# Optimization experiments

Measured on AMD Instinct MI355X. Metric: run time of the kernel, lower is better.

The kernel has to match this reference:

```python
import jax, jax.numpy as jnp
import numpy as np

HEADS = 8
DIM_HEAD = 32


def setup_inputs() -> dict:
    key = jax.random.key(0)
    k1, k2, k3 = jax.random.split(key, 3)
    dim = 256
    hd = HEADS * DIM_HEAD  # 256
    x = jax.random.normal(k1, (2, dim, 16, 64, 64), dtype=jnp.float32)
    w_qkv = jax.random.normal(k2, (3 * hd, dim), dtype=jnp.float32) * (1.0 / np.sqrt(dim))
    w_out = jax.random.normal(k3, (dim, hd), dtype=jnp.float32) * (1.0 / np.sqrt(hd))
    b_out = jnp.zeros((dim,), dtype=jnp.float32)
    return {"x": x, "w_qkv": w_qkv, "w_out": w_out, "b_out": b_out}


def reference(x, w_qkv, w_out, b_out):
    b, c, f, h, w = x.shape
    n = h * w
    scale = DIM_HEAD ** (-0.5)
    # (b c f h w) -> ((b f) c (h w))
    xr = jnp.transpose(x, (0, 2, 1, 3, 4)).reshape(b * f, c, n)
    # 1x1 conv (no bias) == channel GEMM
    qkv = jnp.einsum('oc,bcn->bon', w_qkv, xr)  # (bf, 3*H*D, n)
    q, k, v = jnp.split(qkv, 3, axis=1)
    def heads(t):
        return t.reshape(b * f, HEADS, DIM_HEAD, n)
    q, k, v = heads(q), heads(k), heads(v)
    q = jax.nn.softmax(q, axis=-2) * scale   # softmax over feature dim d
    k = jax.nn.softmax(k, axis=-1)           # softmax over spatial dim n
    context = jnp.einsum('bhdn,bhen->bhde', k, v)   # (bf, H, D, D)
    out = jnp.einsum('bhde,bhdn->bhen', context, q)  # (bf, H, D, n)
    out = out.reshape(b * f, HEADS * DIM_HEAD, n)
    out = jnp.einsum('oc,bcn->bon', w_out, out) + b_out[None, :, None]
    # ((b f) c (h w)) -> (b c f h w)
    out = out.reshape(b, f, c, h, w)
    return jnp.transpose(out, (0, 2, 1, 3, 4))
```

## Files before the change

kernel.cpp:

```cpp
#include <hip/hip_runtime.h>
#include <cmath>


typedef unsigned short u16;
typedef __attribute__((ext_vector_type(4))) unsigned short u16x4;
typedef __attribute__((ext_vector_type(8))) unsigned short u16x8;
typedef __attribute__((ext_vector_type(4))) unsigned int   u32x4;
typedef __attribute__((ext_vector_type(8))) short bf16x8;
typedef __attribute__((ext_vector_type(4))) float f32x4;

#define XCH_STRIDE 65536
#define XB_STRIDE  16777216

__device__ __forceinline__ float bf2f(u16 u) {
    union { unsigned int i; float f; } w; w.i = ((unsigned int)u) << 16; return w.f;
}
__device__ __forceinline__ u16 f2bf(float f) {
    union { float f; unsigned int i; } w; w.f = f;
    return (u16)((w.i + 0x7FFFu + ((w.i >> 16) & 1u)) >> 16);
}
__device__ __forceinline__ void async16(const void* g, void* l) {
    __builtin_amdgcn_global_load_lds(
        (const __attribute__((address_space(1))) unsigned int*)g,
        (__attribute__((address_space(3))) unsigned int*)l, 16, 0, 0);
}

__global__ __launch_bounds__(256) void k_cvt_x(const float* __restrict__ x,
                                               u16* __restrict__ xbf, int fr0)
{
    const int tid = threadIdx.x;
    const int n0 = blockIdx.x * 64;
    const int c0 = blockIdx.y * 64;
    const int fl = blockIdx.z;
    const int frame = fr0 + fl, b = frame >> 4, f = frame & 15;
    const float* xb = x + (size_t)b * XB_STRIDE + (size_t)f * 4096;
    __shared__ float T[64][65];
    const int nn = tid & 63, cq = tid >> 6;
    #pragma unroll
    for (int r = 0; r < 16; ++r) {
        const int cl = r * 4 + cq;
        T[cl][nn] = xb[(size_t)(c0 + cl) * XCH_STRIDE + n0 + nn];
    }
    __syncthreads();
    const int jl = tid >> 2, c16 = (tid & 3) * 16;
    u16* dst = xbf + ((size_t)fl * 4096 + n0 + jl) * 256 + c0 + c16;
    u16x8 a, bv;
    #pragma unroll
    for (int i = 0; i < 8; ++i) a[i] = f2bf(T[c16 + i][jl]);
    #pragma unroll
    for (int i = 0; i < 8; ++i) bv[i] = f2bf(T[c16 + 8 + i][jl]);
    *(u16x8*)dst = a;
    *(u16x8*)(dst + 8) = bv;
}

__global__ __launch_bounds__(256) void k_cvt_w(const float* __restrict__ w,
                                               u16* __restrict__ wbf)
{
    const int i = (blockIdx.x * 256 + threadIdx.x) * 8;
    u16x8 o;
    #pragma unroll
    for (int j = 0; j < 8; ++j) o[j] = f2bf(w[i + j]);
    *(u16x8*)(wbf + i) = o;
}

__global__ __launch_bounds__(256) void k_qkv_mfma(const u16* __restrict__ xbf,
                                                  const u16* __restrict__ wq,
                                                  u16* __restrict__ qkv)
{
    const int tid = threadIdx.x;
    const int lane = tid & 63, wave = tid >> 6;
    const int ln = lane & 15, quad = lane >> 4;
    const int wm = wave & 1, wn = wave >> 1;
    const int j0 = blockIdx.x * 128;
    const int o0 = blockIdx.y * 128;

    __shared__ __align__(16) u16 sm[128 * 136];
    u16* As = sm;
    u16* Bs = sm + 4096;

    f32x4 acc[4][4] = {};
    const int lrow = lane >> 2;
    const int lk8 = (lane & 3) * 8;

    for (int kk = 0; kk < 256; kk += 32) {
        __syncthreads();
        #pragma unroll
        for (int p = 0; p < 2; ++p) {
            const int chunk = wave * 2 + p;
            const int r = chunk * 16 + lrow;
            async16(wq  + (size_t)(o0 + r) * 256 + kk + lk8, As + chunk * 512);
            async16(xbf + (size_t)(j0 + r) * 256 + kk + lk8, Bs + chunk * 512);
        }
        __syncthreads();
        bf16x8 af[4], bfv[4];
        #pragma unroll
        for (int mi = 0; mi < 4; ++mi)
            af[mi] = *(const bf16x8*)&As[(wm * 64 + mi * 16 + ln) * 32 + quad * 8];
        #pragma unroll
        for (int ni = 0; ni < 4; ++ni)
            bfv[ni] = *(const bf16x8*)&Bs[(wn * 64 + ni * 16 + ln) * 32 + quad * 8];
        #pragma unroll
        for (int mi = 0; mi < 4; ++mi)
            #pragma unroll
            for (int ni = 0; ni < 4; ++ni)
                acc[mi][ni] = __builtin_amdgcn_mfma_f32_16x16x32_bf16(
                    af[mi], bfv[ni], acc[mi][ni], 0, 0, 0);
    }

    __syncthreads();
    u16* outl = sm;
    #pragma unroll
    for (int mi = 0; mi < 4; ++mi)
        #pragma unroll
        for (int ni = 0; ni < 4; ++ni) {
            const int jl = wn * 64 + ni * 16 + ln;
            const int ob = wm * 64 + mi * 16 + quad * 4;
            u16x4 u;
            u[0] = f2bf(acc[mi][ni][0]); u[1] = f2bf(acc[mi][ni][1]);
            u[2] = f2bf(acc[mi][ni][2]); u[3] = f2bf(acc[mi][ni][3]);
            *(u16x4*)&outl[jl * 136 + ob] = u;
        }
    __syncthreads();
    #pragma unroll
    for (int r = 0; r < 8; ++r) {
        const int row = r * 16 + (tid >> 4);
        const int cb = (tid & 15) * 8;
        u32x4 v = *(const u32x4*)&outl[row * 136 + cb];
        *(u32x4*)(qkv + (size_t)(j0 + row) * 768 + o0 + cb) = v;
    }
}

__global__ __launch_bounds__(256) void k_softmax_k(u16* __restrict__ qkv)
{
    const int h = blockIdx.x, fl = blockIdx.y;
    const int tid = threadIdx.x;
    u16* base = qkv + (size_t)fl * 4096 * 768 + 256 + h * 32;
    const int d4 = (tid & 7) * 4, jj = tid >> 3;

    __shared__ float red[32 * 33 + 32];
    float* Lm  = red;
    float* Rsc = red + 32 * 33;

    float m[4] = {-1e30f, -1e30f, -1e30f, -1e30f};
    for (int it = 0; it < 128; ++it) {
        const u16x4 u = *(const u16x4*)(base + (size_t)(jj + it * 32) * 768 + d4);
        #pragma unroll
        for (int i = 0; i < 4; ++i) m[i] = fmaxf(m[i], bf2f(u[i]));
    }
    #pragma unroll
    for (int i = 0; i < 4; ++i) Lm[jj * 33 + d4 + i] = m[i];
    __syncthreads();
    if (tid < 32) {
        float M = -1e30f;
        for (int k = 0; k < 32; ++k) M = fmaxf(M, Lm[k * 33 + tid]);
        Rsc[tid] = M;
    }
    __syncthreads();
    float Mv[4];
    #pragma unroll
    for (int i = 0; i < 4; ++i) Mv[i] = Rsc[d4 + i];
    __syncthreads();

    float s[4] = {0.f, 0.f, 0.f, 0.f};
    for (int it = 0; it < 128; ++it) {
        const u16x4 u = *(const u16x4*)(base + (size_t)(jj + it * 32) * 768 + d4);
        #pragma unroll
        for (int i = 0; i < 4; ++i) s[i] += __expf(bf2f(u[i]) - Mv[i]);
    }
    #pragma unroll
    for (int i = 0; i < 4; ++i) Lm[jj * 33 + d4 + i] = s[i];
    __syncthreads();
    if (tid < 32) {
        float S = 0.f;
        for (int k = 0; k < 32; ++k) S += Lm[k * 33 + tid];
        Rsc[tid] = 1.0f / S;
    }
    __syncthreads();
    float Iv[4];
    #pragma unroll
    for (int i = 0; i < 4; ++i) Iv[i] = Rsc[d4 + i];

    for (int it = 0; it < 128; ++it) {
        u16* p = base + (size_t)(jj + it * 32) * 768 + d4;
        u16x4 u = *(const u16x4*)p;
        u16x4 o;
        #pragma unroll
        for (int i = 0; i < 4; ++i) o[i] = f2bf(__expf(bf2f(u[i]) - Mv[i]) * Iv[i]);
        *(u16x4*)p = o;
    }
}

__global__ __launch_bounds__(256) void k_softmax_q(u16* __restrict__ qkv)
{
    const int tid = threadIdx.x;
    const int j = blockIdx.x * 32 + (tid >> 3);
    const int h = tid & 7;
    u16* p = qkv + (size_t)j * 768 + h * 32;
    u16x8 u[4];
    #pragma unroll
    for (int g = 0; g < 4; ++g) u[g] = *(const u16x8*)(p + g * 8);
    float v[32];
    float m = -1e30f;
    #pragma unroll
    for (int g = 0; g < 4; ++g)
        #pragma unroll
        for (int i = 0; i < 8; ++i) { v[g * 8 + i] = bf2f(u[g][i]); m = fmaxf(m, v[g * 8 + i]); }
    float s = 0.f;
    #pragma unroll
    for (int i = 0; i < 32; ++i) { v[i] = __expf(v[i] - m); s += v[i]; }
    const float inv = 0.17677669529663687f / s;
    #pragma unroll
    for (int g = 0; g < 4; ++g) {
        u16x8 o;
        #pragma unroll
        for (int i = 0; i < 8; ++i) o[i] = f2bf(v[g * 8 + i] * inv);
        *(u16x8*)(p + g * 8) = o;
    }
}

__global__ __launch_bounds__(256) void k_context_w2(const u16* __restrict__ qkv,
                                                    const float* __restrict__ w_out,
                                                    u16* __restrict__ w2)
{
    const int h = blockIdx.x, fl = blockIdx.y;
    const int tid = threadIdx.x;
    __shared__ float Ks[64 * 36], Vs[64 * 36], Cs[32 * 33];

    const int d = tid >> 3, e4 = (tid & 7) * 4;
    const int lr = tid >> 2, lc8 = (tid & 3) * 8;
    float acc[4] = {0.f, 0.f, 0.f, 0.f};
    const u16* kcol = qkv + (size_t)fl * 4096 * 768 + 256 + h * 32 + lc8;

    for (int jt = 0; jt < 4096; jt += 64) {
        const u16* kp = kcol + (size_t)(jt + lr) * 768;
        u16x8 ku = *(const u16x8*)kp;
        u16x8 vu = *(const u16x8*)(kp + 256);
        __syncthreads();
        #pragma unroll
        for (int i = 0; i < 8; ++i) {
            Ks[lr * 36 + lc8 + i] = bf2f(ku[i]);
            Vs[lr * 36 + lc8 + i] = bf2f(vu[i]);
        }
        __syncthreads();
        #pragma unroll 8
        for (int jr = 0; jr < 64; ++jr) {
            const float kd = Ks[jr * 36 + d];
            const f32x4 vv = *(const f32x4*)&Vs[jr * 36 + e4];
            acc[0] = fmaf(kd, vv[0], acc[0]);
            acc[1] = fmaf(kd, vv[1], acc[1]);
            acc[2] = fmaf(kd, vv[2], acc[2]);
            acc[3] = fmaf(kd, vv[3], acc[3]);
        }
    }
    __syncthreads();
    #pragma unroll
    for (int i = 0; i < 4; ++i) Cs[d * 33 + e4 + i] = acc[i];
    __syncthreads();

    const int o = tid;
    float a2[32];
    #pragma unroll
    for (int dd = 0; dd < 32; ++dd) a2[dd] = 0.f;
    for (int e = 0; e < 32; ++e) {
        const float wv = w_out[(size_t)o * 256 + h * 32 + e];
        #pragma unroll
        for (int dd = 0; dd < 32; ++dd) a2[dd] = fmaf(wv, Cs[dd * 33 + e], a2[dd]);
    }
    u16* wp = w2 + (size_t)fl * 65536 + (size_t)o * 256 + h * 32;
    #pragma unroll
    for (int g = 0; g < 4; ++g) {
        u16x8 ov;
        #pragma unroll
        for (int i = 0; i < 8; ++i) ov[i] = f2bf(a2[g * 8 + i]);
        *(u16x8*)(wp + g * 8) = ov;
    }
}

__global__ __launch_bounds__(256) void k_out_mfma(const u16* __restrict__ qkv,
                                                  const u16* __restrict__ w2,
                                                  const float* __restrict__ b_out,
                                                  float* __restrict__ out, int fr0)
{
    const int tid = threadIdx.x;
    const int lane = tid & 63, wave = tid >> 6;
    const int ln = lane & 15, quad = lane >> 4;
    const int wm = wave & 1, wn = wave >> 1;
    const int j0 = blockIdx.x * 128;
    const int o0 = blockIdx.y * 128;
    const int fl = j0 >> 12;
    const int frame = fr0 + fl, b = frame >> 4, f = frame & 15;
    const int nb = j0 & 4095;
    const u16* w2f = w2 + (size_t)fl * 65536;

    __shared__ __align__(16) u16 sm[8192];
    u16* As = sm;
    u16* Bs = sm + 4096;

    f32x4 acc[4][4] = {};
    const int lrow = lane >> 2;
    const int lk8 = (lane & 3) * 8;

    for (int kk = 0; kk < 256; kk += 32) {
        __syncthreads();
        #pragma unroll
        for (int p = 0; p < 2; ++p) {
            const int chunk = wave * 2 + p;
            const int r = chunk * 16 + lrow;
            async16(qkv + (size_t)(j0 + r) * 768 + kk + lk8, As + chunk * 512);
            async16(w2f + (size_t)(o0 + r) * 256 + kk + lk8, Bs + chunk * 512);
        }
        __syncthreads();
        bf16x8 af[4], bfv[4];
        #pragma unroll
        for (int mi = 0; mi < 4; ++mi)
            af[mi] = *(const bf16x8*)&As[(wm * 64 + mi * 16 + ln) * 32 + quad * 8];
        #pragma unroll
        for (int ni = 0; ni < 4; ++ni)
            bfv[ni] = *(const bf16x8*)&Bs[(wn * 64 + ni * 16 + ln) * 32 + quad * 8];
        #pragma unroll
        for (int mi = 0; mi < 4; ++mi)
            #pragma unroll
            for (int ni = 0; ni < 4; ++ni)
                acc[mi][ni] = __builtin_amdgcn_mfma_f32_16x16x32_bf16(
                    af[mi], bfv[ni], acc[mi][ni], 0, 0, 0);
    }

    float* obase = out + (size_t)b * XB_STRIDE + (size_t)f * 4096;
    #pragma unroll
    for (int ni = 0; ni < 4; ++ni) {
        const int o = o0 + wn * 64 + ni * 16 + ln;
        const float bias = b_out[o];
        #pragma unroll
        for (int mi = 0; mi < 4; ++mi) {
            const int jn = nb + wm * 64 + mi * 16 + quad * 4;
            f32x4 v = acc[mi][ni];
            v[0] += bias; v[1] += bias; v[2] += bias; v[3] += bias;
            *(f32x4*)(obase + (size_t)o * XCH_STRIDE + jn) = v;
        }
    }
}

extern "C" void kernel_launch(void* const* d_in, const int* in_sizes, int n_in,
                              void* d_out, int out_size, void* d_ws, size_t ws_size,
                              hipStream_t stream)
{
    const float* x     = (const float*)d_in[0];
    const float* w_qkv = (const float*)d_in[1];
    const float* w_out = (const float*)d_in[2];
    const float* b_out = (const float*)d_in[3];
    float* out = (float*)d_out;

    const size_t per_frame = (size_t)4096 * 256 * 2 + (size_t)4096 * 768 * 2 + 65536 * 2;
    const size_t wq_bytes = 768 * 256 * 2;
    int CF = 32;
    while (CF > 1 && (size_t)CF * per_frame + wq_bytes > ws_size) CF >>= 1;

    u16* wq_bf = (u16*)d_ws;
    u16* xbf   = wq_bf + 768 * 256;
    u16* qkv   = xbf + (size_t)CF * 4096 * 256;
    u16* w2    = qkv + (size_t)CF * 4096 * 768;

    k_cvt_w<<<96, 256, 0, stream>>>(w_qkv, wq_bf);
    for (int fr0 = 0; fr0 < 32; fr0 += CF) {
        k_cvt_x    <<<dim3(64, 4, CF), 256, 0, stream>>>(x, xbf, fr0);
        k_qkv_mfma <<<dim3(CF * 32, 6), 256, 0, stream>>>(xbf, wq_bf, qkv);
        k_softmax_k<<<dim3(8, CF),     256, 0, stream>>>(qkv);
        k_softmax_q<<<dim3(CF * 128),  256, 0, stream>>>(qkv);
        k_context_w2<<<dim3(8, CF),    256, 0, stream>>>(qkv, w_out, w2);
        k_out_mfma <<<dim3(CF * 32, 2), 256, 0, stream>>>(qkv, w2, b_out, out, fr0);
    }
}
```

Before: 584.3 us.

## Fuse q-softmax into QKV GEMM epilogue and split k-softmax/context into parallel passes

Applies the q feature-softmax directly in the QKV GEMM epilogue from LDS, which removes the separate k_softmax_q pass over q. The k spatial-softmax no longer normalizes and rewrites k in place. Instead, an online max/sum over 16 spatial chunks gives per-column stats, and the context GEMM applies exp(k-M) on the fly over 16 spatial splits. The 1/S factor is folded in when the partials are reduced in the w2 fold kernel. This raises parallelism from 8 blocks per frame to 16, and it removes a full read-modify-write of k, at the cost of extra kernels and partial-buffer traffic.

```diff
diff --git a/kernel.cpp b/kernel.cpp
--- a/kernel.cpp
+++ b/kernel.cpp
@@ -121,140 +121,176 @@
             *(u16x4*)&outl[jl * 136 + ob] = u;
         }
     __syncthreads();
-    #pragma unroll
-    for (int r = 0; r < 8; ++r) {
-        const int row = r * 16 + (tid >> 4);
-        const int cb = (tid & 15) * 8;
-        u32x4 v = *(const u32x4*)&outl[row * 136 + cb];
-        *(u32x4*)(qkv + (size_t)(j0 + row) * 768 + o0 + cb) = v;
-    }
-}
-
-__global__ __launch_bounds__(256) void k_softmax_k(u16* __restrict__ qkv)
-{
-    const int h = blockIdx.x, fl = blockIdx.y;
-    const int tid = threadIdx.x;
-    u16* base = qkv + (size_t)fl * 4096 * 768 + 256 + h * 32;
-    const int d4 = (tid & 7) * 4, jj = tid >> 3;
-
-    __shared__ float red[32 * 33 + 32];
-    float* Lm  = red;
-    float* Rsc = red + 32 * 33;
-
-    float m[4] = {-1e30f, -1e30f, -1e30f, -1e30f};
-    for (int it = 0; it < 128; ++it) {
-        const u16x4 u = *(const u16x4*)(base + (size_t)(jj + it * 32) * 768 + d4);
-        #pragma unroll
-        for (int i = 0; i < 4; ++i) m[i] = fmaxf(m[i], bf2f(u[i]));
-    }
-    #pragma unroll
-    for (int i = 0; i < 4; ++i) Lm[jj * 33 + d4 + i] = m[i];
+
+    if (blockIdx.y < 2) {
+        #pragma unroll
+        for (int t = 0; t < 2; ++t) {
+            const int idx = t * 256 + tid;
+            const int r = idx >> 2, hh = idx & 3;
+            const u16* p = &outl[r * 136 + hh * 32];
+            float v[32];
+            float m = -1e30f;
+            #pragma unroll
+            for (int g = 0; g < 4; ++g) {
+                u16x8 u = *(const u16x8*)(p + g * 8);
+                #pragma unroll
+                for (int i = 0; i < 8; ++i) {
+                    v[g * 8 + i] = bf2f(u[i]);
+                    m = fmaxf(m, v[g * 8 + i]);
+                }
+            }
+            float s = 0.f;
+            #pragma unroll
+            for (int i = 0; i < 32; ++i) { v[i] = __expf(v[i] - m); s += v[i]; }
+            const float inv = 0.17677669529663687f / s;
+            u16* q = qkv + (size_t)(j0 + r) * 768 + o0 + hh * 32;
+            #pragma unroll
+            for (int g = 0; g < 4; ++g) {
+                u16x8 ov;
+                #pragma unroll
+                for (int i = 0; i < 8; ++i) ov[i] = f2bf(v[g * 8 + i] * inv);
+                *(u16x8*)(q + g * 8) = ov;
+            }
+        }
+    } else {
+        #pragma unroll
+        for (int r = 0; r < 8; ++r) {
+            const int row = r * 16 + (tid >> 4);
+            const int cb = (tid & 15) * 8;
+            u32x4 v = *(const u32x4*)&outl[row * 136 + cb];
+            *(u32x4*)(qkv + (size_t)(j0 + row) * 768 + o0 + cb) = v;
+        }
+    }
+}
+
+__global__ __launch_bounds__(256) void k_kstat1(const u16* __restrict__ qkv,
+                                                float* __restrict__ sp)
+{
+    const int js = blockIdx.x, fl = blockIdx.y;
+    const int tid = threadIdx.x;
+    const int s = tid >> 5, g = tid & 31;
+    const u16* base = qkv + ((size_t)fl * 4096 + js * 256 + s) * 768 + 256 + g * 8;
+    float m[8], sm[8];
+    #pragma unroll
+    for (int i = 0; i < 8; ++i) { m[i] = -1e30f; sm[i] = 0.f; }
+    for (int it = 0; it < 32; ++it) {
+        u16x8 u = *(const u16x8*)(base + (size_t)it * 8 * 768);
+        #pragma unroll
+        for (int i = 0; i < 8; ++i) {
+            float v = bf2f(u[i]);
+            float nm = fmaxf(m[i], v);
+            sm[i] = sm[i] * __expf(m[i] - nm) + __expf(v - nm);
+            m[i] = nm;
+        }
+    }
+    __shared__ float Lm[8][256], Ls[8][256];
+    #pragma unroll
+    for (int i = 0; i < 8; ++i) { Lm[s][g * 8 + i] = m[i]; Ls[s][g * 8 + i] = sm[i]; }
     __syncthreads();
-    if (tid < 32) {
-        float M = -1e30f;
-        for (int k = 0; k < 32; ++k) M = fmaxf(M, Lm[k * 33 + tid]);
-        Rsc[tid] = M;
-    }
-    __syncthreads();
-    float Mv[4];
-    #pragma unroll
-    for (int i = 0; i < 4; ++i) Mv[i] = Rsc[d4 + i];
-    __syncthreads();
-
-    float s[4] = {0.f, 0.f, 0.f, 0.f};
-    for (int it = 0; it < 128; ++it) {
-        const u16x4 u = *(const u16x4*)(base + (size_t)(jj + it * 32) * 768 + d4);
-        #pragma unroll
-        for (int i = 0; i < 4; ++i) s[i] += __expf(bf2f(u[i]) - Mv[i]);
-    }
-    #pragma unroll
-    for (int i = 0; i < 4; ++i) Lm[jj * 33 + d4 + i] = s[i];
-    __syncthreads();
-    if (tid < 32) {
-        float S = 0.f;
-        for (int k = 0; k < 32; ++k) S += Lm[k * 33 + tid];
-        Rsc[tid] = 1.0f / S;
-    }
-    __syncthreads();
-    float Iv[4];
-    #pragma unroll
-    for (int i = 0; i < 4; ++i) Iv[i] = Rsc[d4 + i];
-
-    for (int it = 0; it < 128; ++it) {
-        u16* p = base + (size_t)(jj + it * 32) * 768 + d4;
-        u16x4 u = *(const u16x4*)p;
-        u16x4 o;
-        #pragma unroll
-        for (int i = 0; i < 4; ++i) o[i] = f2bf(__expf(bf2f(u[i]) - Mv[i]) * Iv[i]);
-        *(u16x4*)p = o;
-    }
-}
-
-__global__ __launch_bounds__(256) void k_softmax_q(u16* __restrict__ qkv)
-{
-    const int tid = threadIdx.x;
-    const int j = blockIdx.x * 32 + (tid >> 3);
-    const int h = tid & 7;
-    u16* p = qkv + (size_t)j * 768 + h * 32;
-    u16x8 u[4];
-    #pragma unroll
-    for (int g = 0; g < 4; ++g) u[g] = *(const u16x8*)(p + g * 8);
-    float v[32];
-    float m = -1e30f;
-    #pragma unroll
-    for (int g = 0; g < 4; ++g)
-        #pragma unroll
-        for (int i = 0; i < 8; ++i) { v[g * 8 + i] = bf2f(u[g][i]); m = fmaxf(m, v[g * 8 + i]); }
-    float s = 0.f;
-    #pragma unroll
-    for (int i = 0; i < 32; ++i) { v[i] = __expf(v[i] - m); s += v[i]; }
-    const float inv = 0.17677669529663687f / s;
-    #pragma unroll
-    for (int g = 0; g < 4; ++g) {
-        u16x8 o;
-        #pragma unroll
-        for (int i = 0; i < 8; ++i) o[i] = f2bf(v[g * 8 + i] * inv);
-        *(u16x8*)(p + g * 8) = o;
-    }
-}
-
-__global__ __launch_bounds__(256) void k_context_w2(const u16* __restrict__ qkv,
-                                                    const float* __restrict__ w_out,
-                                                    u16* __restrict__ w2)
-{
-    const int h = blockIdx.x, fl = blockIdx.y;
-    const int tid = threadIdx.x;
-    __shared__ float Ks[64 * 36], Vs[64 * 36], Cs[32 * 33];
-
-    const int d = tid >> 3, e4 = (tid & 7) * 4;
-    const int lr = tid >> 2, lc8 = (tid & 3) * 8;
-    float acc[4] = {0.f, 0.f, 0.f, 0.f};
-    const u16* kcol = qkv + (size_t)fl * 4096 * 768 + 256 + h * 32 + lc8;
-
-    for (int jt = 0; jt < 4096; jt += 64) {
-        const u16* kp = kcol + (size_t)(jt + lr) * 768;
+    const int col = tid;
+    float M = -1e30f;
+    #pragma unroll
+    for (int k = 0; k < 8; ++k) M = fmaxf(M, Lm[k][col]);
+    float S = 0.f;
+    #pragma unroll
+    for (int k = 0; k < 8; ++k) S += Ls[k][col] * __expf(Lm[k][col] - M);
+    float* o = sp + (((size_t)fl * 16 + js) * 256 + col) * 2;
+    o[0] = M; o[1] = S;
+}
+
+__global__ __launch_bounds__(256) void k_kstat2(const float* __restrict__ sp,
+                                                float* __restrict__ stat)
+{
+    const int fl = blockIdx.x, col = threadIdx.x;
+    float mv[16], sv[16];
+    float M = -1e30f;
+    #pragma unroll
+    for (int js = 0; js < 16; ++js) {
+        const float* p = sp + (((size_t)fl * 16 + js) * 256 + col) * 2;
+        mv[js] = p[0]; sv[js] = p[1];
+        M = fmaxf(M, mv[js]);
+    }
+    float S = 0.f;
+    #pragma unroll
+    for (int js = 0; js < 16; ++js) S += sv[js] * __expf(mv[js] - M);
+    float* o = stat + ((size_t)fl * 256 + col) * 2;
+    o[0] = M; o[1] = 1.0f / S;
+}
+
+__global__ __launch_bounds__(256) void k_ctx(const u16* __restrict__ qkv,
+                                             const float* __restrict__ stat,
+                                             float* __restrict__ P)
+{
+    const int js = blockIdx.x, fl = blockIdx.y;
+    const int tid = threadIdx.x;
+    const int ls = tid >> 5, lg = tid & 31;
+    const int h = tid >> 5, dg = (tid >> 3) & 3, eg = tid & 7;
+    const int d0 = dg * 8, e0 = eg * 4;
+
+    float Mg[8];
+    #pragma unroll
+    for (int i = 0; i < 8; ++i) Mg[i] = stat[((size_t)fl * 256 + lg * 8 + i) * 2];
+
+    __shared__ float expk[8][264], vbuf[8][264];
+    f32x4 acc[8] = {};
+    const u16* kbase = qkv + ((size_t)fl * 4096 + js * 256 + ls) * 768 + 256 + lg * 8;
+
+    for (int ch = 0; ch < 32; ++ch) {
+        const u16* kp = kbase + (size_t)ch * 8 * 768;
         u16x8 ku = *(const u16x8*)kp;
         u16x8 vu = *(const u16x8*)(kp + 256);
         __syncthreads();
         #pragma unroll
         for (int i = 0; i < 8; ++i) {
-            Ks[lr * 36 + lc8 + i] = bf2f(ku[i]);
-            Vs[lr * 36 + lc8 + i] = bf2f(vu[i]);
-        }
-        __syncthreads();
-        #pragma unroll 8
-        for (int jr = 0; jr < 64; ++jr) {
-            const float kd = Ks[jr * 36 + d];
-            const f32x4 vv = *(const f32x4*)&Vs[jr * 36 + e4];
-            acc[0] = fmaf(kd, vv[0], acc[0]);
-            acc[1] = fmaf(kd, vv[1], acc[1]);
-            acc[2] = fmaf(kd, vv[2], acc[2]);
-            acc[3] = fmaf(kd, vv[3], acc[3]);
-        }
-    }
-    __syncthreads();
-    #pragma unroll
-    for (int i = 0; i < 4; ++i) Cs[d * 33 + e4 + i] = acc[i];
+            expk[ls][lg * 8 + i] = __expf(bf2f(ku[i]) - Mg[i]);
+            vbuf[ls][lg * 8 + i] = bf2f(vu[i]);
+        }
+        __syncthreads();
+        #pragma unroll
+        for (int rr = 0; rr < 8; ++rr) {
+            f32x4 w0 = *(const f32x4*)&expk[rr][h * 32 + d0];
+            f32x4 w1 = *(const f32x4*)&expk[rr][h * 32 + d0 + 4];
+            f32x4 vv = *(const f32x4*)&vbuf[rr][h * 32 + e0];
+            #pragma unroll
+            for (int ei = 0; ei < 4; ++ei) {
+                acc[0][ei] = fmaf(w0[0], vv[ei], acc[0][ei]);
+                acc[1][ei] = fmaf(w0[1], vv[ei], acc[1][ei]);
+                acc[2][ei] = fmaf(w0[2], vv[ei], acc[2][ei]);
+                acc[3][ei] = fmaf(w0[3], vv[ei], acc[3][ei]);
+                acc[4][ei] = fmaf(w1[0], vv[ei], acc[4][ei]);
+                acc[5][ei] = fmaf(w1[1], vv[ei], acc[5][ei]);
+                acc[6][ei] = fmaf(w1[2], vv[ei], acc[6][ei]);
+                acc[7][ei] = fmaf(w1[3], vv[ei], acc[7][ei]);
+            }
+        }
+    }
+    float* o = P + ((size_t)fl * 16 + js) * 8192 + (h * 32 + d0) * 32 + e0;
+    #pragma unroll
+    for (int di = 0; di < 8; ++di) *(f32x4*)(o + di * 32) = acc[di];
+}
+
+__global__ __launch_bounds__(256) void k_w2fold(const float* __restrict__ P,
+                                                const float* __restrict__ stat,
+                                                const float* __restrict__ w_out,
+                                                u16* __restrict__ w2)
+{
+    const int h = blockIdx.x, fl = blockIdx.y;
+    const int tid = threadIdx.x;
+    __shared__ float Cs[32 * 33];
+
+    const float* p0 = P + (size_t)fl * 16 * 8192 + h * 1024 + tid * 4;
+    f32x4 sum = {0.f, 0.f, 0.f, 0.f};
+    #pragma unroll
+    for (int js = 0; js < 16; ++js) {
+        f32x4 v = *(const f32x4*)(p0 + (size_t)js * 8192);
+        sum[0] += v[0]; sum[1] += v[1]; sum[2] += v[2]; sum[3] += v[3];
+    }
+    const int d = tid >> 3, e4 = (tid & 7) * 4;
+    const float inv = stat[((size_t)fl * 256 + h * 32 + d) * 2 + 1];
+    Cs[d * 33 + e4 + 0] = sum[0] * inv;
+    Cs[d * 33 + e4 + 1] = sum[1] * inv;
+    Cs[d * 33 + e4 + 2] = sum[2] * inv;
+    Cs[d * 33 + e4 + 3] = sum[3] * inv;
     __syncthreads();
 
     const int o = tid;
@@ -350,23 +386,28 @@
     const float* b_out = (const float*)d_in[3];
     float* out = (float*)d_out;
 
-    const size_t per_frame = (size_t)4096 * 256 * 2 + (size_t)4096 * 768 * 2 + 65536 * 2;
+    const size_t per_frame = (size_t)4096 * 256 * 2 + (size_t)4096 * 768 * 2
+                           + 65536 * 2 + 16 * 512 * 4 + 512 * 4 + 16 * 8192 * 4;
     const size_t wq_bytes = 768 * 256 * 2;
     int CF = 32;
     while (CF > 1 && (size_t)CF * per_frame + wq_bytes > ws_size) CF >>= 1;
 
-    u16* wq_bf = (u16*)d_ws;
-    u16* xbf   = wq_bf + 768 * 256;
-    u16* qkv   = xbf + (size_t)CF * 4096 * 256;
-    u16* w2    = qkv + (size_t)CF * 4096 * 768;
+    u16* wq_bf  = (u16*)d_ws;
+    u16* xbf    = wq_bf + 768 * 256;
+    u16* qkv    = xbf + (size_t)CF * 4096 * 256;
+    u16* w2     = qkv + (size_t)CF * 4096 * 768;
+    float* sp   = (float*)(w2 + (size_t)CF * 65536);
+    float* stat = sp + (size_t)CF * 16 * 256 * 2;
+    float* P    = stat + (size_t)CF * 256 * 2;
 
     k_cvt_w<<<96, 256, 0, stream>>>(w_qkv, wq_bf);
     for (int fr0 = 0; fr0 < 32; fr0 += CF) {
-        k_cvt_x    <<<dim3(64, 4, CF), 256, 0, stream>>>(x, xbf, fr0);
-        k_qkv_mfma <<<dim3(CF * 32, 6), 256, 0, stream>>>(xbf, wq_bf, qkv);
-        k_softmax_k<<<dim3(8, CF),     256, 0, stream>>>(qkv);
-        k_softmax_q<<<dim3(CF * 128),  256, 0, stream>>>(qkv);
-        k_context_w2<<<dim3(8, CF),    256, 0, stream>>>(qkv, w_out, w2);
-        k_out_mfma <<<dim3(CF * 32, 2), 256, 0, stream>>>(qkv, w2, b_out, out, fr0);
-    }
-}
+        k_cvt_x   <<<dim3(64, 4, CF), 256, 0, stream>>>(x, xbf, fr0);
+        k_qkv_mfma<<<dim3(CF * 32, 6), 256, 0, stream>>>(xbf, wq_bf, qkv);
+        k_kstat1  <<<dim3(16, CF), 256, 0, stream>>>(qkv, sp);
+        k_kstat2  <<<CF, 256, 0, stream>>>(sp, stat);
+        k_ctx     <<<dim3(16, CF), 256, 0, stream>>>(qkv, stat, P);
+        k_w2fold  <<<dim3(8, CF), 256, 0, stream>>>(P, stat, w_out, w2);
+        k_out_mfma<<<dim3(CF * 32, 2), 256, 0, stream>>>(qkv, w2, b_out, out, fr0);
+    }
+}
```

Result: faster. 485.8 us (-16.9%).
